# Kernel optimization log

Hardware: AMD Instinct MI355X
Metric: run time of the kernel (lower is better)

Reference implementation:

```python
import jax, jax.numpy as jnp
import numpy as np

NUM_HEAD = 16

def setup_inputs() -> dict:
    key = jax.random.key(0)
    ks = jax.random.split(key, 5)
    B, S, E = 2, 2048, 1024
    x = jax.random.normal(ks[0], (B, S, E), dtype=jnp.float32)
    w_qkv = jax.random.normal(ks[1], (3 * E, E), dtype=jnp.float32) * (E ** -0.5)
    b_qkv = jax.random.normal(ks[2], (3 * E,), dtype=jnp.float32) * 0.01
    w_out = jax.random.normal(ks[3], (E, E), dtype=jnp.float32) * (E ** -0.5)
    b_out = jax.random.normal(ks[4], (E,), dtype=jnp.float32) * 0.01
    return {"x": x, "w_qkv": w_qkv, "b_qkv": b_qkv, "w_out": w_out, "b_out": b_out}

def reference(x, w_qkv, b_qkv, w_out, b_out):
    B, S, E = x.shape
    H = NUM_HEAD
    D = E // H
    # fused QKV projection (torch Linear: x @ W^T + b)
    qkv = x @ w_qkv.T + b_qkv                       # [B, S, 3E]
    qkv = qkv.reshape(B, S, 3, H, D).transpose(2, 0, 3, 1, 4)  # [3, B, H, S, D]
    q, k, v = qkv[0], qkv[1], qkv[2]
    # NOTE: source scales by sqrt(embed_size), not sqrt(head_dim)
    scale = jnp.asarray(E, x.dtype) ** 0.5
    att = jnp.einsum('bhqd,bhkd->bhqk', q, k) / scale   # [B, H, S, S]
    # NOTE: source applies softmax over dim=1 (the head axis) — replicated faithfully
    att = jax.nn.softmax(att, axis=1)
    ctx = jnp.einsum('bhqk,bhkd->bhqd', att, v)         # [B, H, S, D]
    ctx = ctx.transpose(0, 2, 1, 3).reshape(B, S, E)    # [B, S, E]
    return ctx @ w_out.T + b_out
```

## Files before the change

### kernel.cpp

```cpp
#include <hip/hip_runtime.h>
#include <hip/hip_bf16.h>
#include <stdint.h>

typedef float  f32x4  __attribute__((ext_vector_type(4)));
typedef short  bf16x8 __attribute__((ext_vector_type(8)));
typedef short  bf16x4 __attribute__((ext_vector_type(4)));
typedef unsigned short u16x8 __attribute__((ext_vector_type(8)));

#define MFMA16(a, b, c) __builtin_amdgcn_mfma_f32_16x16x32_bf16((a), (b), (c), 0, 0, 0)

#if __has_builtin(__builtin_amdgcn_mfma_f32_16x16x16bf16_1k)
#define MFMA16K16(a, b, c) __builtin_amdgcn_mfma_f32_16x16x16bf16_1k((a), (b), (c), 0, 0, 0)
#else
__device__ __forceinline__ f32x4 mfma16k16_asm(bf16x4 a, bf16x4 b, f32x4 c) {
  f32x4 d;
  asm volatile("v_mfma_f32_16x16x16_bf16 %0, %1, %2, %3"
               : "=v"(d) : "v"(a), "v"(b), "v"(c));
  return d;
}
#define MFMA16K16(a, b, c) mfma16k16_asm((a), (b), (c))
#endif

__device__ __forceinline__ void gload16(const void* g, void* l) {
  __builtin_amdgcn_global_load_lds((const __attribute__((address_space(1))) void*)g,
                                   (__attribute__((address_space(3))) void*)l,
                                   16, 0, 0);
}

__device__ __forceinline__ unsigned short bf16bits(float f) {
  __hip_bfloat16 h = __float2bfloat16(f);
  return *(unsigned short*)&h;
}

__device__ __forceinline__ float bf2f(unsigned short u) {
  unsigned int x = ((unsigned int)u) << 16;
  return *(float*)&x;
}

__device__ __forceinline__ void block_sync_lds() {
  asm volatile("s_waitcnt lgkmcnt(0)" ::: "memory");
  __builtin_amdgcn_s_barrier();
  asm volatile("" ::: "memory");
}

__global__ void cast_kernel(const float* __restrict__ s, __hip_bfloat16* __restrict__ d, int n4) {
  int i = blockIdx.x * blockDim.x + threadIdx.x;
  if (i < n4) {
    float4 v = ((const float4*)s)[i];
    ushort4 u;
    u.x = bf16bits(v.x); u.y = bf16bits(v.y); u.z = bf16bits(v.z); u.w = bf16bits(v.w);
    ((ushort4*)d)[i] = u;
  }
}

__global__ __launch_bounds__(256) void gemm_qkv_kernel(
    const __hip_bfloat16* __restrict__ A,
    const __hip_bfloat16* __restrict__ B,
    const float* __restrict__ bias,
    __hip_bfloat16* __restrict__ Qo,
    __hip_bfloat16* __restrict__ Ko,
    __hip_bfloat16* __restrict__ Vt) {
  const int K = 1024;
  __shared__ __align__(16) __hip_bfloat16 As[128 * 32];
  __shared__ __align__(16) __hip_bfloat16 Bs[128 * 32];
  const int t = threadIdx.x;
  const int lane = t & 63, wv = t >> 6;
  const int wm = (wv >> 1) * 64, wn = (wv & 1) * 64;
  const int lr = lane & 15, lq = lane >> 4;
  const int m0 = blockIdx.y * 128, n0 = blockIdx.x * 128;

  f32x4 acc[4][4] = {};

  const int arow = t >> 2;
  const int acol = (t & 3) * 8;
  const __hip_bfloat16* Ag = A + (long)(m0 + arow) * K + acol;
  const __hip_bfloat16* Bg = B + (long)(n0 + arow) * K + acol;
  __hip_bfloat16* Asl = As + t * 8;
  __hip_bfloat16* Bsl = Bs + t * 8;

  for (int kk = 0; kk < K; kk += 32) {
    gload16(Ag + kk, Asl);
    gload16(Ag + kk + 64 * K, Asl + 2048);
    gload16(Bg + kk, Bsl);
    gload16(Bg + kk + 64 * K, Bsl + 2048);
    __syncthreads();
    bf16x8 af[4], bf[4];
#pragma unroll
    for (int i = 0; i < 4; ++i)
      af[i] = *(const bf16x8*)&As[(wm + i * 16 + lr) * 32 + lq * 8];
#pragma unroll
    for (int j = 0; j < 4; ++j)
      bf[j] = *(const bf16x8*)&Bs[(wn + j * 16 + lr) * 32 + lq * 8];
#pragma unroll
    for (int i = 0; i < 4; ++i)
#pragma unroll
      for (int j = 0; j < 4; ++j)
        acc[i][j] = MFMA16(af[i], bf[j], acc[i][j]);
    __syncthreads();
  }

#pragma unroll
  for (int i = 0; i < 4; ++i) {
#pragma unroll
    for (int j = 0; j < 4; ++j) {
      int col = n0 + wn + j * 16 + lr;
      int tsel = col >> 10, rem = col & 1023;
      int h = rem >> 6, d = rem & 63;
      float bs = bias[col];
      int rowb = m0 + wm + i * 16 + lq * 4;
#pragma unroll
      for (int r = 0; r < 4; ++r) {
        int m = rowb + r;
        int b = m >> 11, sdx = m & 2047;
        __hip_bfloat16 v = __float2bfloat16(acc[i][j][r] + bs);
        long bh = (long)(b * 16 + h);
        if (tsel == 0) {
          Qo[(bh * 2048 + sdx) * 64 + d] = v;
        } else if (tsel == 1) {
          Ko[(bh * 128 + (sdx >> 4)) * 1024 + (d >> 5) * 512 +
             ((d >> 3) & 3) * 128 + (sdx & 15) * 8 + (d & 7)] = v;
        } else {
          Vt[((bh * 128 + (sdx >> 4)) * 64 + d) * 16 + (sdx & 15)] = v;
        }
      }
    }
  }
}

__global__ __launch_bounds__(512, 2) void attn_kernel(
    const __hip_bfloat16* __restrict__ Q,
    const __hip_bfloat16* __restrict__ K,
    const __hip_bfloat16* __restrict__ Vt,
    __hip_bfloat16* __restrict__ part) {
  __shared__ float psum[2][5120];
  __shared__ __align__(16) unsigned short epi[16 * 1024];

  const int t = threadIdx.x, lane = t & 63, wv = t >> 6;
  const int lr = lane & 15, lq = lane >> 4;
  const int h0 = wv * 2;
  const int combo = blockIdx.x & 7;
  const int b = combo & 1, chunk = combo >> 1;
  const int q0 = (blockIdx.x >> 3) * 32;
  const int kb0 = chunk * 32;
  const float c = 0.03125f * 1.44269504f;
  const long bh16 = (long)(b * 16);
  const int poff = lr * 20 + lq * 4;

  bf16x8 qf[2][2][2];
#pragma unroll
  for (int hh = 0; hh < 2; ++hh)
#pragma unroll
    for (int qt = 0; qt < 2; ++qt)
#pragma unroll
      for (int dh = 0; dh < 2; ++dh)
        qf[hh][qt][dh] = *(const bf16x8*)(
            Q + ((bh16 + h0 + hh) * 2048 + q0 + qt * 16 + lr) * 64 + dh * 32 + lq * 8);

  bf16x8 kfA[2][2], kfB[2][2];
  bf16x4 vgA[2][4], vgB[2][4];

  auto loadKV = [&](bf16x8 (&KF)[2][2], bf16x4 (&VG)[2][4], int kb) {
#pragma unroll
    for (int hh = 0; hh < 2; ++hh) {
      const __hip_bfloat16* kptr =
          K + ((bh16 + h0 + hh) * 128 + kb) * 1024 + lq * 128 + lr * 8;
      KF[hh][0] = *(const bf16x8*)kptr;
      KF[hh][1] = *(const bf16x8*)(kptr + 512);
      const __hip_bfloat16* vptr =
          Vt + ((bh16 + h0 + hh) * 128 + kb) * 1024 + lr * 16 + lq * 4;
#pragma unroll
      for (int dt = 0; dt < 4; ++dt)
        VG[hh][dt] = *(const bf16x4*)(vptr + dt * 256);
    }
  };

  loadKV(kfA, vgA, kb0);

  f32x4 ctx[2][2][4] = {};

  auto body = [&](bf16x8 (&KF)[2][2], bf16x4 (&VG)[2][4],
                  bf16x8 (&KFN)[2][2], bf16x4 (&VGN)[2][4], int kt, int par) {
    f32x4 s[2][2];
    __builtin_amdgcn_s_setprio(1);
#pragma unroll
    for (int hh = 0; hh < 2; ++hh)
#pragma unroll
      for (int qt = 0; qt < 2; ++qt) {
        f32x4 a = {};
        a = MFMA16(KF[hh][0], qf[hh][qt][0], a);
        a = MFMA16(KF[hh][1], qf[hh][qt][1], a);
        s[hh][qt] = a;
      }
    __builtin_amdgcn_s_setprio(0);
    if (kt + 1 < 32) loadKV(KFN, VGN, kb0 + kt + 1);
#pragma unroll
    for (int qt = 0; qt < 2; ++qt) {
      f32x4 pp;
#pragma unroll
      for (int r = 0; r < 4; ++r) {
        s[0][qt][r] = __builtin_amdgcn_exp2f(s[0][qt][r] * c);
        s[1][qt][r] = __builtin_amdgcn_exp2f(s[1][qt][r] * c);
        pp[r] = s[0][qt][r] + s[1][qt][r];
      }
      *(f32x4*)&psum[par][qt * 2560 + wv * 320 + poff] = pp;
    }
    block_sync_lds();
    f32x4 inv[2];
#pragma unroll
    for (int qt = 0; qt < 2; ++qt) {
      f32x4 tot = {};
#pragma unroll
      for (int w2 = 0; w2 < 8; ++w2)
        tot += *(const f32x4*)&psum[par][qt * 2560 + w2 * 320 + poff];
#pragma unroll
      for (int r = 0; r < 4; ++r) inv[qt][r] = __builtin_amdgcn_rcpf(tot[r]);
    }
    __builtin_amdgcn_s_setprio(1);
#pragma unroll
    for (int hh = 0; hh < 2; ++hh)
#pragma unroll
      for (int qt = 0; qt < 2; ++qt) {
        bf16x4 p4;
#pragma unroll
        for (int r = 0; r < 4; ++r) p4[r] = (short)bf16bits(s[hh][qt][r] * inv[qt][r]);
#pragma unroll
        for (int dt = 0; dt < 4; ++dt)
          ctx[hh][qt][dt] = MFMA16K16(VG[hh][dt], p4, ctx[hh][qt][dt]);
      }
    __builtin_amdgcn_s_setprio(0);
  };

#pragma unroll 1
  for (int kp = 0; kp < 16; ++kp) {
    body(kfA, vgA, kfB, vgB, 2 * kp, 0);
    body(kfB, vgB, kfA, vgA, 2 * kp + 1, 1);
  }

  unsigned short* Pc = epi;
#pragma unroll
  for (int qt = 0; qt < 2; ++qt) {
    if (qt) block_sync_lds();
#pragma unroll
    for (int hh = 0; hh < 2; ++hh) {
      const int h = h0 + hh;
#pragma unroll
      for (int dt = 0; dt < 4; ++dt) {
        bf16x4 pk;
#pragma unroll
        for (int r = 0; r < 4; ++r) pk[r] = (short)bf16bits(ctx[hh][qt][dt][r]);
        const int o = h * 128 + dt * 32 + lq * 8;
        *(bf16x4*)((char*)Pc + lr * 2048 + (o ^ ((lr & 7) << 4))) = pk;
      }
    }
    block_sync_lds();
    unsigned short* gbase = (unsigned short*)part +
        ((long)(chunk * 4096 + b * 2048 + q0 + qt * 16)) * 1024;
#pragma unroll
    for (int j = 0; j < 4; ++j) {
      int gf = (j * 512 + t) * 8;
      int q = gf >> 10, hd = gf & 1023;
      u16x8 v = *(const u16x8*)((char*)Pc + q * 2048 + ((hd * 2) ^ ((q & 7) << 4)));
      *(u16x8*)&gbase[gf] = v;
    }
  }
}

__global__ void reduce_cast_kernel(const unsigned short* __restrict__ part,
                                   __hip_bfloat16* __restrict__ dst) {
  int i = blockIdx.x * blockDim.x + threadIdx.x;
  const long S4 = (long)4096 * 1024 / 4;
  const ushort4* p = (const ushort4*)part;
  float sx = 0.f, sy = 0.f, sz = 0.f, sw = 0.f;
#pragma unroll
  for (int c = 0; c < 4; ++c) {
    ushort4 v = p[i + c * S4];
    sx += bf2f(v.x); sy += bf2f(v.y); sz += bf2f(v.z); sw += bf2f(v.w);
  }
  ushort4 u;
  u.x = bf16bits(sx); u.y = bf16bits(sy); u.z = bf16bits(sz); u.w = bf16bits(sw);
  ((ushort4*)dst)[i] = u;
}

__global__ __launch_bounds__(256) void gemm_out_kernel(
    const __hip_bfloat16* __restrict__ A,
    const __hip_bfloat16* __restrict__ B,
    const float* __restrict__ bias,
    float* __restrict__ out) {
  const int K = 1024;
  __shared__ __align__(16) __hip_bfloat16 As[128 * 32];
  __shared__ __align__(16) __hip_bfloat16 Bs[128 * 32];
  const int t = threadIdx.x;
  const int lane = t & 63, wv = t >> 6;
  const int wm = (wv >> 1) * 64, wn = (wv & 1) * 64;
  const int lr = lane & 15, lq = lane >> 4;
  const int m0 = blockIdx.y * 128, n0 = blockIdx.x * 128;

  f32x4 acc[4][4] = {};

  const int arow = t >> 2;
  const int acol = (t & 3) * 8;
  const __hip_bfloat16* Ag = A + (long)(m0 + arow) * K + acol;
  const __hip_bfloat16* Bg = B + (long)(n0 + arow) * K + acol;
  __hip_bfloat16* Asl = As + t * 8;
  __hip_bfloat16* Bsl = Bs + t * 8;

  for (int kk = 0; kk < K; kk += 32) {
    gload16(Ag + kk, Asl);
    gload16(Ag + kk + 64 * K, Asl + 2048);
    gload16(Bg + kk, Bsl);
    gload16(Bg + kk + 64 * K, Bsl + 2048);
    __syncthreads();
    bf16x8 af[4], bf[4];
#pragma unroll
    for (int i = 0; i < 4; ++i)
      af[i] = *(const bf16x8*)&As[(wm + i * 16 + lr) * 32 + lq * 8];
#pragma unroll
    for (int j = 0; j < 4; ++j)
      bf[j] = *(const bf16x8*)&Bs[(wn + j * 16 + lr) * 32 + lq * 8];
#pragma unroll
    for (int i = 0; i < 4; ++i)
#pragma unroll
      for (int j = 0; j < 4; ++j)
        acc[i][j] = MFMA16(af[i], bf[j], acc[i][j]);
    __syncthreads();
  }

#pragma unroll
  for (int i = 0; i < 4; ++i) {
#pragma unroll
    for (int j = 0; j < 4; ++j) {
      int col = n0 + wn + j * 16 + lr;
      float bs = bias[col];
      int rowb = m0 + wm + i * 16 + lq * 4;
#pragma unroll
      for (int r = 0; r < 4; ++r) {
        out[(long)(rowb + r) * 1024 + col] = acc[i][j][r] + bs;
      }
    }
  }
}

extern "C" void kernel_launch(void* const* d_in, const int* in_sizes, int n_in,
                              void* d_out, int out_size, void* d_ws, size_t ws_size,
                              hipStream_t stream) {
  const float* x     = (const float*)d_in[0];
  const float* w_qkv = (const float*)d_in[1];
  const float* b_qkv = (const float*)d_in[2];
  const float* w_out = (const float*)d_in[3];
  const float* b_out = (const float*)d_in[4];
  float* out = (float*)d_out;
  char* ws = (char*)d_ws;

  __hip_bfloat16* xb    = (__hip_bfloat16*)(ws);
  __hip_bfloat16* wqkvb = (__hip_bfloat16*)(ws + (8ul << 20));
  __hip_bfloat16* woutb = (__hip_bfloat16*)(ws + (14ul << 20));
  __hip_bfloat16* Qb    = (__hip_bfloat16*)(ws + (16ul << 20));
  __hip_bfloat16* Kb    = (__hip_bfloat16*)(ws + (24ul << 20));
  __hip_bfloat16* Vtb   = (__hip_bfloat16*)(ws + (32ul << 20));
  __hip_bfloat16* partb = (__hip_bfloat16*)(ws + (40ul << 20));
  __hip_bfloat16* ctxb  = (__hip_bfloat16*)(ws + (72ul << 20));

  cast_kernel<<<4096, 256, 0, stream>>>(x, xb, 4194304 / 4);
  cast_kernel<<<3072, 256, 0, stream>>>(w_qkv, wqkvb, 3145728 / 4);
  cast_kernel<<<1024, 256, 0, stream>>>(w_out, woutb, 1048576 / 4);
  gemm_qkv_kernel<<<dim3(24, 32), 256, 0, stream>>>(xb, wqkvb, b_qkv, Qb, Kb, Vtb);
  attn_kernel<<<512, 512, 0, stream>>>(Qb, Kb, Vtb, partb);
  reduce_cast_kernel<<<4096, 256, 0, stream>>>((const unsigned short*)partb, ctxb);
  gemm_out_kernel<<<dim3(8, 32), 256, 0, stream>>>(ctxb, woutb, b_out, out);
}
```

Measured before the change: 290.8 us.

## Software-pipeline attention PV step one tile behind and split head-sum reduction

Restructures the attention inner loop so the P·V MFMA for tile t-1 runs after the QK^T and exp of tile t, splitting K and V loads so V prefetch happens later. The cross-head softmax denominator is now reduced cooperatively: each lane sums one column across the 8 waves and writes a reciprocal to shared memory, instead of every lane summing 8 f32x4 vectors. This is meant to cut redundant LDS reads and hide the barrier latency behind MFMA work. In exchange it adds a trailing epilogue step, more live registers for the two score buffers, and a slightly larger shared buffer.

```diff
diff --git a/kernel.cpp b/kernel.cpp
--- a/kernel.cpp
+++ b/kernel.cpp
@@ -132,7 +132,7 @@
     const __hip_bfloat16* __restrict__ K,
     const __hip_bfloat16* __restrict__ Vt,
     __hip_bfloat16* __restrict__ part) {
-  __shared__ float psum[2][5120];
+  __shared__ float psum[2][5760];
   __shared__ __align__(16) unsigned short epi[16 * 1024];
 
   const int t = threadIdx.x, lane = t & 63, wv = t >> 6;
@@ -145,6 +145,7 @@
   const float c = 0.03125f * 1.44269504f;
   const long bh16 = (long)(b * 16);
   const int poff = lr * 20 + lq * 4;
+  const int roff = (lane >> 5) * 320 + (wv * 2 + ((lane >> 4) & 1)) * 20 + (lane & 15);
 
   bf16x8 qf[2][2][2];
 #pragma unroll
@@ -159,13 +160,18 @@
   bf16x8 kfA[2][2], kfB[2][2];
   bf16x4 vgA[2][4], vgB[2][4];
 
-  auto loadKV = [&](bf16x8 (&KF)[2][2], bf16x4 (&VG)[2][4], int kb) {
+  auto loadK = [&](bf16x8 (&KF)[2][2], int kb) {
 #pragma unroll
     for (int hh = 0; hh < 2; ++hh) {
       const __hip_bfloat16* kptr =
           K + ((bh16 + h0 + hh) * 128 + kb) * 1024 + lq * 128 + lr * 8;
       KF[hh][0] = *(const bf16x8*)kptr;
       KF[hh][1] = *(const bf16x8*)(kptr + 512);
+    }
+  };
+  auto loadV = [&](bf16x4 (&VG)[2][4], int kb) {
+#pragma unroll
+    for (int hh = 0; hh < 2; ++hh) {
       const __hip_bfloat16* vptr =
           Vt + ((bh16 + h0 + hh) * 128 + kb) * 1024 + lr * 16 + lq * 4;
 #pragma unroll
@@ -174,66 +180,90 @@
     }
   };
 
-  loadKV(kfA, vgA, kb0);
+  loadK(kfA, kb0);
+  loadV(vgA, kb0);
 
   f32x4 ctx[2][2][4] = {};
-
-  auto body = [&](bf16x8 (&KF)[2][2], bf16x4 (&VG)[2][4],
-                  bf16x8 (&KFN)[2][2], bf16x4 (&VGN)[2][4], int kt, int par) {
-    f32x4 s[2][2];
+  f32x4 sA[2][2], sB[2][2];
+
+  auto body = [&](bf16x8 (&KFc)[2][2], bf16x8 (&KFn)[2][2],
+                  f32x4 (&Sc)[2][2], f32x4 (&Sp)[2][2],
+                  bf16x4 (&VGp)[2][4], int tt, int par) {
     __builtin_amdgcn_s_setprio(1);
 #pragma unroll
     for (int hh = 0; hh < 2; ++hh)
 #pragma unroll
       for (int qt = 0; qt < 2; ++qt) {
         f32x4 a = {};
-        a = MFMA16(KF[hh][0], qf[hh][qt][0], a);
-        a = MFMA16(KF[hh][1], qf[hh][qt][1], a);
-        s[hh][qt] = a;
+        a = MFMA16(KFc[hh][0], qf[hh][qt][0], a);
+        a = MFMA16(KFc[hh][1], qf[hh][qt][1], a);
+        Sc[hh][qt] = a;
       }
     __builtin_amdgcn_s_setprio(0);
-    if (kt + 1 < 32) loadKV(KFN, VGN, kb0 + kt + 1);
+    if (tt + 1 < 32) loadK(KFn, kb0 + tt + 1);
 #pragma unroll
     for (int qt = 0; qt < 2; ++qt) {
       f32x4 pp;
 #pragma unroll
       for (int r = 0; r < 4; ++r) {
-        s[0][qt][r] = __builtin_amdgcn_exp2f(s[0][qt][r] * c);
-        s[1][qt][r] = __builtin_amdgcn_exp2f(s[1][qt][r] * c);
-        pp[r] = s[0][qt][r] + s[1][qt][r];
-      }
-      *(f32x4*)&psum[par][qt * 2560 + wv * 320 + poff] = pp;
+        Sc[0][qt][r] = __builtin_amdgcn_exp2f(Sc[0][qt][r] * c);
+        Sc[1][qt][r] = __builtin_amdgcn_exp2f(Sc[1][qt][r] * c);
+        pp[r] = Sc[0][qt][r] + Sc[1][qt][r];
+      }
+      *(f32x4*)&psum[par][wv * 640 + qt * 320 + poff] = pp;
     }
     block_sync_lds();
-    f32x4 inv[2];
-#pragma unroll
-    for (int qt = 0; qt < 2; ++qt) {
-      f32x4 tot = {};
-#pragma unroll
-      for (int w2 = 0; w2 < 8; ++w2)
-        tot += *(const f32x4*)&psum[par][qt * 2560 + w2 * 320 + poff];
-#pragma unroll
-      for (int r = 0; r < 4; ++r) inv[qt][r] = __builtin_amdgcn_rcpf(tot[r]);
-    }
-    __builtin_amdgcn_s_setprio(1);
-#pragma unroll
-    for (int hh = 0; hh < 2; ++hh)
-#pragma unroll
-      for (int qt = 0; qt < 2; ++qt) {
-        bf16x4 p4;
-#pragma unroll
-        for (int r = 0; r < 4; ++r) p4[r] = (short)bf16bits(s[hh][qt][r] * inv[qt][r]);
-#pragma unroll
-        for (int dt = 0; dt < 4; ++dt)
-          ctx[hh][qt][dt] = MFMA16K16(VG[hh][dt], p4, ctx[hh][qt][dt]);
-      }
-    __builtin_amdgcn_s_setprio(0);
+    {
+      float tot = 0.f;
+#pragma unroll
+      for (int w2 = 0; w2 < 8; ++w2) tot += psum[par][w2 * 640 + roff];
+      psum[par][5120 + roff] = __builtin_amdgcn_rcpf(tot);
+    }
+    if (tt > 0) {
+      f32x4 inv0 = *(const f32x4*)&psum[par ^ 1][5120 + poff];
+      f32x4 inv1 = *(const f32x4*)&psum[par ^ 1][5120 + 320 + poff];
+      __builtin_amdgcn_s_setprio(1);
+#pragma unroll
+      for (int hh = 0; hh < 2; ++hh)
+#pragma unroll
+        for (int qt = 0; qt < 2; ++qt) {
+          const f32x4 iv = qt ? inv1 : inv0;
+          bf16x4 p4;
+#pragma unroll
+          for (int r = 0; r < 4; ++r) p4[r] = (short)bf16bits(Sp[hh][qt][r] * iv[r]);
+#pragma unroll
+          for (int dt = 0; dt < 4; ++dt)
+            ctx[hh][qt][dt] = MFMA16K16(VGp[hh][dt], p4, ctx[hh][qt][dt]);
+        }
+      __builtin_amdgcn_s_setprio(0);
+    }
+    if (tt + 1 < 32) loadV(VGp, kb0 + tt + 1);
   };
 
 #pragma unroll 1
   for (int kp = 0; kp < 16; ++kp) {
-    body(kfA, vgA, kfB, vgB, 2 * kp, 0);
-    body(kfB, vgB, kfA, vgA, 2 * kp + 1, 1);
+    body(kfA, kfB, sA, sB, vgB, 2 * kp, 0);
+    body(kfB, kfA, sB, sA, vgA, 2 * kp + 1, 1);
+  }
+
+  block_sync_lds();
+  {
+    f32x4 inv0 = *(const f32x4*)&psum[1][5120 + poff];
+    f32x4 inv1 = *(const f32x4*)&psum[1][5120 + 320 + poff];
+    __builtin_amdgcn_s_setprio(1);
+#pragma unroll
+    for (int hh = 0; hh < 2; ++hh)
+#pragma unroll
+      for (int qt = 0; qt < 2; ++qt) {
+        const f32x4 iv = qt ? inv1 : inv0;
+        bf16x4 p4;
+#pragma unroll
+        for (int r = 0; r < 4; ++r) p4[r] = (short)bf16bits(sB[hh][qt][r] * iv[r]);
+#pragma unroll
+        for (int dt = 0; dt < 4; ++dt)
+          ctx[hh][qt][dt] = MFMA16K16(vgB[hh][dt], p4, ctx[hh][qt][dt]);
+      }
+    __builtin_amdgcn_s_setprio(0);
   }
 
   unsigned short* Pc = epi;
```

Result: faster. 272.1 us (-6.4%).
